# Performance work log

Hardware: AMD Instinct MI355X
Metric: run time of the kernel (lower is better)

Reference implementation:

```python
import jax, jax.numpy as jnp
import numpy as np

B, C, T = 128, 19, 1000

def _conv2d(x, w, pad, groups=1):
    return jax.lax.conv_general_dilated(x, w, (1, 1), [(pad[0], pad[0]), (pad[1], pad[1])],
                                        dimension_numbers=('NCHW', 'OIHW', 'NCHW'),
                                        feature_group_count=groups)

def _conv1d(x, w, pad):
    return jax.lax.conv_general_dilated(x, w, (1,), [(pad, pad)],
                                        dimension_numbers=('NCH', 'OIH', 'NCH'))

def _bn(x, g, b, axis=1):
    # eval-mode BatchNorm with running_mean=0, running_var=1 -> pure affine
    shp = [1] * x.ndim
    shp[axis] = -1
    return x * g.reshape(shp) + b.reshape(shp)

def _gat(x, W, a_src, a_dst, bias, src, dst, ew):
    # GATConv, concat=False (head mean); messages scaled by external edge weight ew
    N = x.shape[0]
    H, D = a_src.shape
    h = (x @ W).reshape(N, H, D)
    e = jax.nn.leaky_relu((h * a_src).sum(-1)[src] + (h * a_dst).sum(-1)[dst], 0.2)  # [E,H]
    emax = jax.ops.segment_max(e, dst, num_segments=N)
    ee = jnp.exp(e - emax[dst])
    alpha = ee / (jax.ops.segment_sum(ee, dst, num_segments=N)[dst] + 1e-16)
    msg = (alpha * ew[:, None])[:, :, None] * h[src]  # [E,H,D]
    return jax.ops.segment_sum(msg, dst, num_segments=N).mean(1) + bias

def setup_inputs():
    key = jax.random.key(0)
    ks = iter(jax.random.split(key, 48))
    def nrm(shape, s=0.1):
        return jax.random.normal(next(ks), shape, jnp.float32) * s
    ii = np.arange(C)
    base = np.arange(B)[:, None] * C
    src = (base + np.repeat(ii, C)[None, :]).reshape(-1)
    dst = (base + np.tile(ii, C)[None, :]).reshape(-1)
    return {
        'x': nrm((B, C, T), 1.0),
        'conv1_w': nrm((16, 1, 1, 25)),
        'bn1_g': 1.0 + nrm((16,)), 'bn1_b': nrm((16,)),
        'depth_w': nrm((16, 1, C, 1)),
        'bn2_g': 1.0 + nrm((16,)), 'bn2_b': nrm((16,)),
        'se_w1': nrm((16, 4)), 'se_w2': nrm((4, 16)),
        'sep_w': nrm((16, 16, 1, 16)),
        'bn3_g': 1.0 + nrm((16,)), 'bn3_b': nrm((16,)),
        'ms_w0': nrm((16, 1, 15)), 'ms_g0': 1.0 + nrm((16,)), 'ms_b0': nrm((16,)),
        'ms_w1': nrm((16, 1, 25)), 'ms_g1': 1.0 + nrm((16,)), 'ms_b1': nrm((16,)),
        'ms_w2': nrm((16, 1, 35)), 'ms_g2': 1.0 + nrm((16,)), 'ms_b2': nrm((16,)),
        'adj_w': nrm((32, 1)), 'adj_b': nrm((1,)),
        'gat1_w': nrm((32, 8 * 64), 0.05), 'gat1_as': nrm((8, 64)), 'gat1_ad': nrm((8, 64)), 'gat1_bias': nrm((64,)),
        'skip1_w': nrm((32, 64)), 'skip1_b': nrm((64,)),
        'bng1_g': 1.0 + nrm((64,)), 'bng1_b': nrm((64,)),
        'gat2_w': nrm((64, 8 * 64), 0.05), 'gat2_as': nrm((8, 64)), 'gat2_ad': nrm((8, 64)), 'gat2_bias': nrm((64,)),
        'bng2_g': 1.0 + nrm((64,)), 'bng2_b': nrm((64,)),
        'cls_w1': nrm((64, 64)), 'cls_b1': nrm((64,)),
        'cls_w2': nrm((64, 2)), 'cls_b2': nrm((2,)),
        'edge_index': jnp.asarray(np.stack([src, dst]), dtype=jnp.int32),
        'batch_idx': jnp.repeat(jnp.arange(B, dtype=jnp.int32), C),
    }

def reference(x, conv1_w, bn1_g, bn1_b, depth_w, bn2_g, bn2_b, se_w1, se_w2, sep_w, bn3_g, bn3_b,
              ms_w0, ms_g0, ms_b0, ms_w1, ms_g1, ms_b1, ms_w2, ms_g2, ms_b2,
              adj_w, adj_b, gat1_w, gat1_as, gat1_ad, gat1_bias, skip1_w, skip1_b, bng1_g, bng1_b,
              gat2_w, gat2_as, gat2_ad, gat2_bias, bng2_g, bng2_b, cls_w1, cls_b1, cls_w2, cls_b2,
              edge_index, batch_idx):
    Bn, Cn, Tn = x.shape
    gelu = lambda v: jax.nn.gelu(v, approximate=False)
    # --- EEGNet-style frontend ---
    y = _conv2d(x[:, None], conv1_w, (0, 12))                 # [B,16,C,T]
    y = _bn(y, bn1_g, bn1_b)
    y = _conv2d(y, depth_w, (0, 0), groups=16)                # depthwise over channels -> [B,16,1,T]
    y = jax.nn.elu(_bn(y, bn2_g, bn2_b))
    s = y.mean((2, 3))                                        # SE squeeze [B,16]
    s = jax.nn.sigmoid(gelu(s @ se_w1) @ se_w2)
    y = y * s[:, :, None, None]
    y = y.reshape(Bn, 16, 1, Tn // 4, 4).mean(-1)             # AvgPool2d((1,4))
    y = jax.nn.elu(_bn(_conv2d(y, sep_w, (0, 8)), bn3_g, bn3_b))
    yv = y.mean((2, 3))                                       # AdaptiveAvgPool2d((C,1)): 1->C replicates
    y_nodes = jnp.broadcast_to(yv[:, None, :], (Bn, Cn, 16)).reshape(Bn * Cn, 16)
    # --- per-channel multiscale conv1d ---
    z = x.reshape(Bn * Cn, 1, Tn)
    acc = jax.nn.elu(_bn(_conv1d(z, ms_w0, 7), ms_g0, ms_b0))
    acc = acc + jax.nn.elu(_bn(_conv1d(z, ms_w1, 12), ms_g1, ms_b1))
    acc = acc + jax.nn.elu(_bn(_conv1d(z, ms_w2, 17), ms_g2, ms_b2))
    z = (acc / 3.0).mean(-1)                                  # AdaptiveAvgPool1d(1) -> [N,16]
    feat = jnp.concatenate([y_nodes, z], axis=1)              # [N,32]
    # --- edge-weighted GAT stack ---
    scores = jax.nn.sigmoid(feat @ adj_w + adj_b).reshape(-1)
    src, dst = edge_index[0], edge_index[1]
    ew = scores[src] * scores[dst]
    h = _gat(feat, gat1_w, gat1_as, gat1_ad, gat1_bias, src, dst, ew)
    h = gelu(_bn(h, bng1_g, bng1_b) + feat @ skip1_w + skip1_b)
    h2 = _gat(h, gat2_w, gat2_as, gat2_ad, gat2_bias, src, dst, ew)
    h = gelu(_bn(h2, bng2_g, bng2_b) + h2)
    # --- global mean pool + classifier ---
    gs = jax.ops.segment_sum(h, batch_idx, num_segments=Bn)
    cnt = jax.ops.segment_sum(jnp.ones((Bn * Cn, 1), h.dtype), batch_idx, num_segments=Bn)
    g = gs / cnt
    return gelu(g @ cls_w1 + cls_b1) @ cls_w2 + cls_b2
```

## Files before the change

kernel.cpp:

```cpp
#include <hip/hip_runtime.h>
#include <hip/hip_bf16.h>
#include <math.h>

#define BATCH 128
#define NCH 19
#define TLEN 1000
#define NNODES (BATCH * NCH)

__device__ __forceinline__ float eluf(float x) { return x > 0.f ? x : __expf(x) - 1.f; }
__device__ __forceinline__ float geluf(float x) { return 0.5f * x * (1.f + erff(x * 0.70710678118654752f)); }
__device__ __forceinline__ float sigf(float x) { return 1.f / (1.f + __expf(-x)); }
__device__ __forceinline__ float lrelu(float x) { return x > 0.f ? x : 0.2f * x; }

__global__ __launch_bounds__(256) void k_pool(
    const float* __restrict__ x, const float* __restrict__ w1,
    const float* __restrict__ bn1g, const float* __restrict__ bn1b,
    const float* __restrict__ dw, const float* __restrict__ bn2g,
    const float* __restrict__ bn2b, float* __restrict__ y4g,
    float* __restrict__ ssum) {
  int blk = blockIdx.x;
  int b = blk >> 4, f = blk & 15;
  int tid = threadIdx.x;
  __shared__ float xw[1024];
  __shared__ float dws[19], w1s[25];
  __shared__ float redw[4];
  if (tid < 19) dws[tid] = dw[f * 19 + tid];
  else if (tid >= 32 && tid < 57) w1s[tid - 32] = w1[f * 25 + tid - 32];
  __syncthreads();
  const float* xb = x + (size_t)b * NCH * TLEN;
  for (int i = tid; i < 1024; i += 256) {
    int t = i - 12;
    float v = 0.f;
    if (t >= 0 && t < TLEN) {
#pragma unroll
      for (int c = 0; c < 19; c++) v += dws[c] * xb[c * TLEN + t];
    }
    xw[i] = v;
  }
  __syncthreads();
  float g1 = bn1g[f], b1 = bn1b[f];
  float g2 = bn2g[f], b2 = bn2b[f];
  float sumdw = 0.f;
#pragma unroll
  for (int c = 0; c < 19; c++) sumdw += dws[c];
  float scale = g2 * g1, cb = g2 * b1 * sumdw + b2;
  float part = 0.f;
  if (tid < 250) {
    float pool = 0.f;
#pragma unroll
    for (int q = 0; q < 4; q++) {
      int t = 4 * tid + q;
      float acc = 0.f;
#pragma unroll
      for (int k = 0; k < 25; k++) acc += w1s[k] * xw[t + k];
      pool += eluf(scale * acc + cb);
    }
    part = pool;
    y4g[(size_t)(b * 16 + f) * 250 + tid] = pool * 0.25f;
  }
  int lane = tid & 63, wid = tid >> 6;
  for (int off = 32; off > 0; off >>= 1) part += __shfl_down(part, off, 64);
  if (lane == 0) redw[wid] = part;
  __syncthreads();
  if (tid == 0) ssum[b * 16 + f] = redw[0] + redw[1] + redw[2] + redw[3];
}

__global__ __launch_bounds__(256) void k_sep(
    const float* __restrict__ y4g, const float* __restrict__ ssum,
    const float* __restrict__ sew1, const float* __restrict__ sew2,
    const float* __restrict__ sw, const float* __restrict__ g3,
    const float* __restrict__ b3, float* __restrict__ yv) {
  int blk = blockIdx.x;
  int b = blk >> 4, fo = blk & 15;
  int tid = threadIdx.x;
  __shared__ float yloc[16 * 268];
  __shared__ float sws[256];
  __shared__ float s_s[16], se_s[16], u4[4];
  __shared__ float redw[4];
  sws[tid] = sw[fo * 256 + tid];
  if (tid < 16) s_s[tid] = ssum[b * 16 + tid] * (1.f / 1000.f);
  __syncthreads();
  if (tid < 4) {
    float a = 0.f;
#pragma unroll
    for (int ff = 0; ff < 16; ff++) a += s_s[ff] * sew1[ff * 4 + tid];
    u4[tid] = geluf(a);
  }
  __syncthreads();
  if (tid < 16) {
    float a = 0.f;
#pragma unroll
    for (int j = 0; j < 4; j++) a += u4[j] * sew2[j * 16 + tid];
    se_s[tid] = sigf(a);
  }
  __syncthreads();
#pragma unroll
  for (int fi = 0; fi < 16; fi++) {
    float sc = se_s[fi];
    const float* yr = y4g + (size_t)(b * 16 + fi) * 250;
    for (int j = tid; j < 268; j += 256) {
      float v = (j >= 8 && j < 258) ? yr[j - 8] * sc : 0.f;
      yloc[fi * 268 + j] = v;
    }
  }
  __syncthreads();
  float accsum = 0.f;
  if (tid < 251) {
    float acc = 0.f;
#pragma unroll
    for (int fi = 0; fi < 16; fi++) {
      const float* yr = &yloc[fi * 268 + tid];
      const float* wp = &sws[fi * 16];
#pragma unroll
      for (int k = 0; k < 16; k++) acc += yr[k] * wp[k];
    }
    accsum = eluf(g3[fo] * acc + b3[fo]);
  }
  int lane = tid & 63, wid = tid >> 6;
  for (int off = 32; off > 0; off >>= 1)
    accsum += __shfl_down(accsum, off, 64);
  if (lane == 0) redw[wid] = accsum;
  __syncthreads();
  if (tid == 0)
    yv[b * 16 + fo] = (redw[0] + redw[1] + redw[2] + redw[3]) * (1.f / 251.f);
}

#define RP 8
__global__ __launch_bounds__(256) void k_ms(
    const float* __restrict__ x, const float* __restrict__ w0,
    const float* __restrict__ ga0, const float* __restrict__ bb0,
    const float* __restrict__ w1, const float* __restrict__ ga1,
    const float* __restrict__ bb1, const float* __restrict__ w2,
    const float* __restrict__ ga2, const float* __restrict__ bb2,
    const float* __restrict__ yv, float* __restrict__ feat) {
  int n = blockIdx.x, tid = threadIdx.x;
  __shared__ float xr[1034];
  __shared__ float wst[1200];
  __shared__ float red[256];
  for (int i = tid; i < 1034; i += 256) {
    int t = i - 17;
    xr[i] = (t >= 0 && t < TLEN) ? x[(size_t)n * TLEN + t] : 0.f;
  }
  for (int i = tid; i < 240; i += 256) wst[i] = w0[i];
  for (int i = tid; i < 400; i += 256) wst[240 + i] = w1[i];
  for (int i = tid; i < 560; i += 256) wst[640 + i] = w2[i];
  __syncthreads();

  int f = tid & 15, plane = tid >> 4;
  float wa[15], wb[25], wc[35];
#pragma unroll
  for (int k = 0; k < 15; k++) wa[k] = wst[f * 15 + k];
#pragma unroll
  for (int k = 0; k < 25; k++) wb[k] = wst[240 + f * 25 + k];
#pragma unroll
  for (int k = 0; k < 35; k++) wc[k] = wst[640 + f * 35 + k];
  float g0 = ga0[f], c0 = bb0[f];
  float g1 = ga1[f], c1 = bb1[f];
  float g2 = ga2[f], c2 = bb2[f];

  float z = 0.f;
  for (int base = plane * RP; base < TLEN; base += 16 * RP) {
    float xv[34 + RP];
#pragma unroll
    for (int i = 0; i < 34 + RP; i++) xv[i] = xr[base + i];
#pragma unroll
    for (int r = 0; r < RP; r++) {
      float a0 = 0.f, a1 = 0.f, a2 = 0.f;
#pragma unroll
      for (int k = 0; k < 15; k++) a0 += xv[r + 10 + k] * wa[k];
#pragma unroll
      for (int k = 0; k < 25; k++) a1 += xv[r + 5 + k] * wb[k];
#pragma unroll
      for (int k = 0; k < 35; k++) a2 += xv[r + k] * wc[k];
      z += eluf(g0 * a0 + c0) + eluf(g1 * a1 + c1) + eluf(g2 * a2 + c2);
    }
  }
  red[tid] = z;
  __syncthreads();
  for (int s = 128; s >= 16; s >>= 1) {
    if (tid < s) red[tid] += red[tid + s];
    __syncthreads();
  }
  if (tid < 16) {
    feat[(size_t)n * 32 + 16 + tid] = red[tid] * (1.f / 3000.f);
    feat[(size_t)n * 32 + tid] = yv[(n / 19) * 16 + tid];
  }
}

__global__ __launch_bounds__(256) void k_gat(
    const float* __restrict__ feat, const float* __restrict__ adjw,
    const float* __restrict__ adjb, const float* __restrict__ g1w,
    const float* __restrict__ g1as, const float* __restrict__ g1ad,
    const float* __restrict__ g1bias, const float* __restrict__ skw,
    const float* __restrict__ skb, const float* __restrict__ bg1,
    const float* __restrict__ bb1, const float* __restrict__ g2w,
    const float* __restrict__ g2as, const float* __restrict__ g2ad,
    const float* __restrict__ g2bias, const float* __restrict__ bg2,
    const float* __restrict__ bb2, const float* __restrict__ cw1,
    const float* __restrict__ cb1, const float* __restrict__ cw2,
    const float* __restrict__ cb2, float* __restrict__ out) {
  int b = blockIdx.x, tid = threadIdx.x;
  __shared__ float fb[19 * 32];
  __shared__ float h1[19 * 512];
  __shared__ float as_s[19 * 8], ad_s[19 * 8], sc_s[19];
  __shared__ float watt[19 * 8 * 19];
  __shared__ float hb[19 * 64];
  __shared__ float hout[19 * 64];
  __shared__ float gpool[64], u_s[64];

  for (int i = tid; i < 19 * 32; i += 256) fb[i] = feat[(size_t)b * 19 * 32 + i];
  __syncthreads();

  {
    float wc0[32], wc1[32];
#pragma unroll
    for (int c = 0; c < 32; c++) {
      wc0[c] = g1w[c * 512 + tid];
      wc1[c] = g1w[c * 512 + tid + 256];
    }
    for (int i = 0; i < 19; i++) {
      float frow[32];
#pragma unroll
      for (int c = 0; c < 32; c++) frow[c] = fb[i * 32 + c];
      float a0 = 0.f, a1 = 0.f;
#pragma unroll
      for (int c = 0; c < 32; c++) {
        a0 += frow[c] * wc0[c];
        a1 += frow[c] * wc1[c];
      }
      h1[i * 512 + tid] = a0;
      h1[i * 512 + tid + 256] = a1;
    }
  }
  if (tid < 19) {
    float a = adjb[0];
#pragma unroll
    for (int c = 0; c < 32; c++) a += fb[tid * 32 + c] * adjw[c];
    sc_s[tid] = sigf(a);
  }
  __syncthreads();

  if (tid < 152) {
    int i = tid / 8, h = tid & 7;
    float a = 0.f, d2 = 0.f;
#pragma unroll
    for (int d = 0; d < 64; d++) {
      float hv = h1[i * 512 + h * 64 + d];
      a += hv * g1as[h * 64 + d];
      d2 += hv * g1ad[h * 64 + d];
    }
    as_s[tid] = a;
    ad_s[tid] = d2;
  }
  __syncthreads();
  if (tid < 152) {
    int j = tid / 8, h = tid & 7;
    float adj_ = ad_s[j * 8 + h];
    float ev[19], m = -1e30f;
#pragma unroll
    for (int i = 0; i < 19; i++) {
      float e = lrelu(as_s[i * 8 + h] + adj_);
      ev[i] = e;
      m = fmaxf(m, e);
    }
    float den = 0.f;
#pragma unroll
    for (int i = 0; i < 19; i++) {
      ev[i] = __expf(ev[i] - m);
      den += ev[i];
    }
    float inv = 1.f / (den + 1e-16f);
    float scj = sc_s[j];
#pragma unroll
    for (int i = 0; i < 19; i++)
      watt[(j * 8 + h) * 19 + i] = ev[i] * inv * sc_s[i] * scj;
  }
  __syncthreads();
  for (int idx = tid; idx < 19 * 64; idx += 256) {
    int j = idx >> 6, d = idx & 63;
    float acc = 0.f;
#pragma unroll
    for (int h = 0; h < 8; h++) {
      const float* wr = &watt[(j * 8 + h) * 19];
      float a = 0.f;
#pragma unroll
      for (int i = 0; i < 19; i++) a += wr[i] * h1[i * 512 + h * 64 + d];
      acc += a;
    }
    float om = acc * 0.125f + g1bias[d];
    float v = bg1[d] * om + bb1[d];
    float sk = skb[d];
    const float* fr = &fb[j * 32];
#pragma unroll
    for (int c = 0; c < 32; c++) sk += fr[c] * skw[c * 64 + d];
    hb[idx] = geluf(v + sk);
  }
  __syncthreads();

#pragma unroll
  for (int oo = 0; oo < 2; oo++) {
    int o = tid + oo * 256;
    float wc[64];
#pragma unroll
    for (int c = 0; c < 64; c++) wc[c] = g2w[c * 512 + o];
    for (int i = 0; i < 19; i++) {
      float a = 0.f;
#pragma unroll
      for (int c = 0; c < 64; c++) a += hb[i * 64 + c] * wc[c];
      h1[i * 512 + o] = a;
    }
  }
  __syncthreads();

  if (tid < 152) {
    int i = tid / 8, h = tid & 7;
    float a = 0.f, d2 = 0.f;
#pragma unroll
    for (int d = 0; d < 64; d++) {
      float hv = h1[i * 512 + h * 64 + d];
      a += hv * g2as[h * 64 + d];
      d2 += hv * g2ad[h * 64 + d];
    }
    as_s[tid] = a;
    ad_s[tid] = d2;
  }
  __syncthreads();
  if (tid < 152) {
    int j = tid / 8, h = tid & 7;
    float adj_ = ad_s[j * 8 + h];
    float ev[19], m = -1e30f;
#pragma unroll
    for (int i = 0; i < 19; i++) {
      float e = lrelu(as_s[i * 8 + h] + adj_);
      ev[i] = e;
      m = fmaxf(m, e);
    }
    float den = 0.f;
#pragma unroll
    for (int i = 0; i < 19; i++) {
      ev[i] = __expf(ev[i] - m);
      den += ev[i];
    }
    float inv = 1.f / (den + 1e-16f);
    float scj = sc_s[j];
#pragma unroll
    for (int i = 0; i < 19; i++)
      watt[(j * 8 + h) * 19 + i] = ev[i] * inv * sc_s[i] * scj;
  }
  __syncthreads();
  for (int idx = tid; idx < 19 * 64; idx += 256) {
    int j = idx >> 6, d = idx & 63;
    float acc = 0.f;
#pragma unroll
    for (int h = 0; h < 8; h++) {
      const float* wr = &watt[(j * 8 + h) * 19];
      float a = 0.f;
#pragma unroll
      for (int i = 0; i < 19; i++) a += wr[i] * h1[i * 512 + h * 64 + d];
      acc += a;
    }
    float om = acc * 0.125f + g2bias[d];
    float v = bg2[d] * om + bb2[d] + om;
    hout[idx] = geluf(v);
  }
  __syncthreads();

  if (tid < 64) {
    float a = 0.f;
#pragma unroll
    for (int j = 0; j < 19; j++) a += hout[j * 64 + tid];
    gpool[tid] = a * (1.f / 19.f);
  }
  __syncthreads();
  if (tid < 64) {
    float a = cb1[tid];
#pragma unroll
    for (int d = 0; d < 64; d++) a += gpool[d] * cw1[d * 64 + tid];
    u_s[tid] = geluf(a);
  }
  __syncthreads();
  if (tid < 2) {
    float a = cb2[tid];
#pragma unroll
    for (int e = 0; e < 64; e++) a += u_s[e] * cw2[e * 2 + tid];
    out[b * 2 + tid] = a;
  }
}

extern "C" void kernel_launch(void* const* d_in, const int* in_sizes, int n_in,
                              void* d_out, int out_size, void* d_ws,
                              size_t ws_size, hipStream_t stream) {
  (void)in_sizes; (void)n_in; (void)out_size; (void)ws_size;
  const float* x = (const float*)d_in[0];
  const float* conv1_w = (const float*)d_in[1];
  const float* bn1_g = (const float*)d_in[2];
  const float* bn1_b = (const float*)d_in[3];
  const float* depth_w = (const float*)d_in[4];
  const float* bn2_g = (const float*)d_in[5];
  const float* bn2_b = (const float*)d_in[6];
  const float* se_w1 = (const float*)d_in[7];
  const float* se_w2 = (const float*)d_in[8];
  const float* sep_w = (const float*)d_in[9];
  const float* bn3_g = (const float*)d_in[10];
  const float* bn3_b = (const float*)d_in[11];
  const float* ms_w0 = (const float*)d_in[12];
  const float* ms_g0 = (const float*)d_in[13];
  const float* ms_b0 = (const float*)d_in[14];
  const float* ms_w1 = (const float*)d_in[15];
  const float* ms_g1 = (const float*)d_in[16];
  const float* ms_b1 = (const float*)d_in[17];
  const float* ms_w2 = (const float*)d_in[18];
  const float* ms_g2 = (const float*)d_in[19];
  const float* ms_b2 = (const float*)d_in[20];
  const float* adj_w = (const float*)d_in[21];
  const float* adj_b = (const float*)d_in[22];
  const float* gat1_w = (const float*)d_in[23];
  const float* gat1_as = (const float*)d_in[24];
  const float* gat1_ad = (const float*)d_in[25];
  const float* gat1_bias = (const float*)d_in[26];
  const float* skip1_w = (const float*)d_in[27];
  const float* skip1_b = (const float*)d_in[28];
  const float* bng1_g = (const float*)d_in[29];
  const float* bng1_b = (const float*)d_in[30];
  const float* gat2_w = (const float*)d_in[31];
  const float* gat2_as = (const float*)d_in[32];
  const float* gat2_ad = (const float*)d_in[33];
  const float* gat2_bias = (const float*)d_in[34];
  const float* bng2_g = (const float*)d_in[35];
  const float* bng2_b = (const float*)d_in[36];
  const float* cls_w1 = (const float*)d_in[37];
  const float* cls_b1 = (const float*)d_in[38];
  const float* cls_w2 = (const float*)d_in[39];
  const float* cls_b2 = (const float*)d_in[40];

  float* ws = (float*)d_ws;
  float* yv = ws;
  float* feat = ws + 2048;
  float* y4g = ws + 79872;
  float* ssum = ws + 591872;

  hipLaunchKernelGGL(k_pool, dim3(BATCH * 16), dim3(256), 0, stream,
                     x, conv1_w, bn1_g, bn1_b, depth_w, bn2_g, bn2_b, y4g, ssum);
  hipLaunchKernelGGL(k_sep, dim3(BATCH * 16), dim3(256), 0, stream,
                     y4g, ssum, se_w1, se_w2, sep_w, bn3_g, bn3_b, yv);
  hipLaunchKernelGGL(k_ms, dim3(NNODES), dim3(256), 0, stream,
                     x, ms_w0, ms_g0, ms_b0, ms_w1, ms_g1, ms_b1, ms_w2,
                     ms_g2, ms_b2, yv, feat);
  hipLaunchKernelGGL(k_gat, dim3(BATCH), dim3(256), 0, stream,
                     feat, adj_w, adj_b, gat1_w, gat1_as, gat1_ad, gat1_bias,
                     skip1_w, skip1_b, bng1_g, bng1_b, gat2_w, gat2_as,
                     gat2_ad, gat2_bias, bng2_g, bng2_b, cls_w1, cls_b1,
                     cls_w2, cls_b2, (float*)d_out);
}
```

Baseline: 378.7 us.

## Remap multiscale conv so each wavefront handles filters with uniform scalar weights

Reassigns work in the multiscale conv1d kernel so each wavefront processes four filters in sequence, with every lane covering four time steps. Because the filter index is wave-uniform (readfirstlane), weights can be loaded as scalar values instead of per-lane registers from shared memory. Input windows are read from shared memory as float4 vectors. The shared-memory tree reduction is replaced by wave shuffles. The cost is more redundant input loading per filter and a tail guard on the last chunk.

```diff
diff --git a/kernel.cpp b/kernel.cpp
--- a/kernel.cpp
+++ b/kernel.cpp
@@ -125,7 +125,6 @@
     yv[b * 16 + fo] = (redw[0] + redw[1] + redw[2] + redw[3]) * (1.f / 251.f);
 }
 
-#define RP 8
 __global__ __launch_bounds__(256) void k_ms(
     const float* __restrict__ x, const float* __restrict__ w0,
     const float* __restrict__ ga0, const float* __restrict__ bb0,
@@ -134,55 +133,62 @@
     const float* __restrict__ ga2, const float* __restrict__ bb2,
     const float* __restrict__ yv, float* __restrict__ feat) {
   int n = blockIdx.x, tid = threadIdx.x;
-  __shared__ float xr[1034];
-  __shared__ float wst[1200];
-  __shared__ float red[256];
-  for (int i = tid; i < 1034; i += 256) {
+  int lane = tid & 63, wid = tid >> 6;
+  __shared__ __align__(16) float xr[1040];
+  __shared__ float red_s[16];
+  for (int i = tid; i < 1040; i += 256) {
     int t = i - 17;
     xr[i] = (t >= 0 && t < TLEN) ? x[(size_t)n * TLEN + t] : 0.f;
   }
-  for (int i = tid; i < 240; i += 256) wst[i] = w0[i];
-  for (int i = tid; i < 400; i += 256) wst[240 + i] = w1[i];
-  for (int i = tid; i < 560; i += 256) wst[640 + i] = w2[i];
-  __syncthreads();
-
-  int f = tid & 15, plane = tid >> 4;
-  float wa[15], wb[25], wc[35];
-#pragma unroll
-  for (int k = 0; k < 15; k++) wa[k] = wst[f * 15 + k];
-#pragma unroll
-  for (int k = 0; k < 25; k++) wb[k] = wst[240 + f * 25 + k];
-#pragma unroll
-  for (int k = 0; k < 35; k++) wc[k] = wst[640 + f * 35 + k];
-  float g0 = ga0[f], c0 = bb0[f];
-  float g1 = ga1[f], c1 = bb1[f];
-  float g2 = ga2[f], c2 = bb2[f];
-
-  float z = 0.f;
-  for (int base = plane * RP; base < TLEN; base += 16 * RP) {
-    float xv[34 + RP];
-#pragma unroll
-    for (int i = 0; i < 34 + RP; i++) xv[i] = xr[base + i];
-#pragma unroll
-    for (int r = 0; r < RP; r++) {
-      float a0 = 0.f, a1 = 0.f, a2 = 0.f;
-#pragma unroll
-      for (int k = 0; k < 15; k++) a0 += xv[r + 10 + k] * wa[k];
-#pragma unroll
-      for (int k = 0; k < 25; k++) a1 += xv[r + 5 + k] * wb[k];
-#pragma unroll
-      for (int k = 0; k < 35; k++) a2 += xv[r + k] * wc[k];
-      z += eluf(g0 * a0 + c0) + eluf(g1 * a1 + c1) + eluf(g2 * a2 + c2);
-    }
-  }
-  red[tid] = z;
-  __syncthreads();
-  for (int s = 128; s >= 16; s >>= 1) {
-    if (tid < s) red[tid] += red[tid + s];
-    __syncthreads();
-  }
+  __syncthreads();
+
+  for (int fg = 0; fg < 4; fg++) {
+    int fu = __builtin_amdgcn_readfirstlane(wid * 4 + fg);
+    float wa[15], wb[25], wc[35];
+#pragma unroll
+    for (int k = 0; k < 15; k++) wa[k] = w0[fu * 15 + k];
+#pragma unroll
+    for (int k = 0; k < 25; k++) wb[k] = w1[fu * 25 + k];
+#pragma unroll
+    for (int k = 0; k < 35; k++) wc[k] = w2[fu * 35 + k];
+    float g0 = ga0[fu], c0 = bb0[fu];
+    float g1 = ga1[fu], c1 = bb1[fu];
+    float g2 = ga2[fu], c2 = bb2[fu];
+
+    float z = 0.f;
+    for (int tb = 0; tb < TLEN; tb += 256) {
+      int t0 = tb + lane * 4;
+      int rb = t0 <= 996 ? t0 : 996;
+      float4 xq[10];
+      const float4* xp = reinterpret_cast<const float4*>(&xr[rb]);
+#pragma unroll
+      for (int i = 0; i < 10; i++) xq[i] = xp[i];
+      float xv[40];
+#pragma unroll
+      for (int i = 0; i < 10; i++) {
+        xv[4 * i] = xq[i].x; xv[4 * i + 1] = xq[i].y;
+        xv[4 * i + 2] = xq[i].z; xv[4 * i + 3] = xq[i].w;
+      }
+#pragma unroll
+      for (int q = 0; q < 4; q++) {
+        if (t0 + q < TLEN) {
+          float a0 = 0.f, a1 = 0.f, a2 = 0.f;
+#pragma unroll
+          for (int k = 0; k < 15; k++) a0 += xv[q + 10 + k] * wa[k];
+#pragma unroll
+          for (int k = 0; k < 25; k++) a1 += xv[q + 5 + k] * wb[k];
+#pragma unroll
+          for (int k = 0; k < 35; k++) a2 += xv[q + k] * wc[k];
+          z += eluf(g0 * a0 + c0) + eluf(g1 * a1 + c1) + eluf(g2 * a2 + c2);
+        }
+      }
+    }
+    for (int off = 32; off > 0; off >>= 1) z += __shfl_down(z, off, 64);
+    if (lane == 0) red_s[fu] = z;
+  }
+  __syncthreads();
   if (tid < 16) {
-    feat[(size_t)n * 32 + 16 + tid] = red[tid] * (1.f / 3000.f);
+    feat[(size_t)n * 32 + 16 + tid] = red_s[tid] * (1.f / 3000.f);
     feat[(size_t)n * 32 + tid] = yv[(n / 19) * 16 + tid];
   }
 }
```

New measurement: 407.3 us. 1.08x slower.
